# Performance work log

Hardware: AMD Instinct MI355X
Metric: run time of the kernel (lower is better)

## Reference

```python
import jax, jax.numpy as jnp
import numpy as np

N = 512          # Cartesian grid size (nRead)
C = 16           # n_coils
K = 262144       # n non-uniform k-space samples (~512 spokes x 512 readouts)


def setup_inputs() -> dict:
    key = jax.random.key(0)
    ks = jax.random.split(key, 6)
    x_real = jax.random.normal(ks[0], (C, K), jnp.float32)
    x_imag = jax.random.normal(ks[1], (C, K), jnp.float32)
    csm_real = jax.random.normal(ks[2], (C, N, N), jnp.float32)
    csm_imag = jax.random.normal(ks[3], (C, N, N), jnp.float32)
    # normalized k-space coordinates in [-0.5, 0.5)
    traj = jax.random.uniform(ks[4], (K, 2), jnp.float32, -0.5, 0.5)
    # density compensation weights (positive)
    dcf = jax.random.uniform(ks[5], (K,), jnp.float32)
    return dict(x_real=x_real, x_imag=x_imag, csm_real=csm_real,
                csm_imag=csm_imag, traj=traj, dcf=dcf)


def reference(x_real, x_imag, csm_real, csm_imag, traj, dcf):
    # Adjoint gridding NUFFT with density compensation + coil-sensitivity combine.
    # 1) density-compensate the multicoil non-Cartesian samples
    x = (x_real + 1j * x_imag) * dcf                      # [C, K] complex64
    # 2) grid (scatter-add) onto the Cartesian k-space grid (nearest-cell gridding)
    t = jax.lax.stop_gradient(traj)
    idx = jnp.round((t + 0.5) * N).astype(jnp.int32) % N  # [K, 2]
    iy, ix = idx[:, 0], idx[:, 1]
    grid = jnp.zeros((C, N, N), jnp.complex64).at[:, iy, ix].add(x)
    # 3) centered inverse FFT to image space (adjoint of DFT, scaled by N^2)
    img = jnp.fft.fftshift(
        jnp.fft.ifft2(jnp.fft.ifftshift(grid, axes=(-2, -1)), axes=(-2, -1)),
        axes=(-2, -1)) * (N * N)                          # [C, N, N]
    # 4) coil combine with conjugate sensitivity maps
    csm = csm_real + 1j * csm_imag
    out = jnp.sum(jnp.conj(csm) * img, axis=0)            # [N, N] complex64
    # return real/imag stacked, with batch dim (mimics numpy2tensor add_batch_dim)
    return jnp.stack([out.real, out.imag])[None]          # [1, 2, N, N]
```

## Files before the change

kernel.cpp:

```cpp
#include <hip/hip_runtime.h>
#include <math.h>

#define N 512
#define NN (N * N)
#define C 16
#define K 262144
#define LOG2N 9
#define NCOL 8

#define SK(e) ((e) + ((e) >> 4))
#define LROW 544


__global__ __launch_bounds__(256) void prep_hist_kernel(const float2* __restrict__ traj,
                                                        const float* __restrict__ dcf,
                                                        int* __restrict__ cell,
                                                        float* __restrict__ sdcf,
                                                        int* __restrict__ count) {
    int k = blockIdx.x * 256 + threadIdx.x;
    float2 t = traj[k];
    int iy = __float2int_rn((t.x + 0.5f) * (float)N) & (N - 1);
    int ix = __float2int_rn((t.y + 0.5f) * (float)N) & (N - 1);
    int cl = iy * N + ix;
    cell[k] = cl;
    float s = ((iy + ix) & 1) ? -1.0f : 1.0f;
    sdcf[k] = dcf[k] * s;
    atomicAdd(&count[cl], 1);
}

__global__ __launch_bounds__(256) void scan_reduce_kernel(const int* __restrict__ count,
                                                          int* __restrict__ bsum) {
    __shared__ int sd[256];
    int t = threadIdx.x;
    const int4* c4 = (const int4*)count;
    int4 v = c4[blockIdx.x * 256 + t];
    sd[t] = v.x + v.y + v.z + v.w;
    __syncthreads();
    for (int d = 128; d > 0; d >>= 1) {
        if (t < d) sd[t] += sd[t + d];
        __syncthreads();
    }
    if (t == 0) bsum[blockIdx.x] = sd[0];
}

__global__ __launch_bounds__(256) void scan_top_kernel(const int* __restrict__ bsum,
                                                       int* __restrict__ boffs,
                                                       int* __restrict__ offs) {
    __shared__ int sd[256];
    int t = threadIdx.x;
    int v = bsum[t];
    sd[t] = v;
    __syncthreads();
    for (int d = 1; d < 256; d <<= 1) {
        int tmp = (t >= d) ? sd[t - d] : 0;
        __syncthreads();
        sd[t] += tmp;
        __syncthreads();
    }
    boffs[t] = sd[t] - v;
    if (t == 0) offs[NN] = K;
}

__global__ __launch_bounds__(256) void scan_final_kernel(const int* __restrict__ count,
                                                         const int* __restrict__ boffs,
                                                         int* __restrict__ offs,
                                                         int* __restrict__ cursor) {
    __shared__ int sd[256];
    int t = threadIdx.x;
    int base_idx = blockIdx.x * 256 + t;
    const int4* c4 = (const int4*)count;
    int4 v = c4[base_idx];
    int s = v.x + v.y + v.z + v.w;
    sd[t] = s;
    __syncthreads();
    for (int d = 1; d < 256; d <<= 1) {
        int tmp = (t >= d) ? sd[t - d] : 0;
        __syncthreads();
        sd[t] += tmp;
        __syncthreads();
    }
    int base = boffs[blockIdx.x] + sd[t] - s;
    int4 o;
    o.x = base;
    o.y = base + v.x;
    o.z = base + v.x + v.y;
    o.w = base + v.x + v.y + v.z;
    ((int4*)offs)[base_idx] = o;
    ((int4*)cursor)[base_idx] = o;
}

__global__ __launch_bounds__(256) void payload_kernel(const float* __restrict__ xr,
                                                      const float* __restrict__ xi,
                                                      const int* __restrict__ cell,
                                                      const float* __restrict__ sdcf,
                                                      int* __restrict__ cursor,
                                                      float2* __restrict__ payA,
                                                      float2* __restrict__ payB) {
    __shared__ float tR[256][17];
    __shared__ float tI[256][17];
    __shared__ int   sp[256];
    __shared__ float sw[256];
    int t = threadIdx.x;
    int k0 = blockIdx.x * 256;
#pragma unroll
    for (int c = 0; c < C; ++c) {
        tR[t][c] = xr[(size_t)c * K + k0 + t];
        tI[t][c] = xi[(size_t)c * K + k0 + t];
    }
    int cl = cell[k0 + t];
    float w = sdcf[k0 + t];
    int p = atomicAdd(&cursor[cl], 1);
    sp[t] = p;
    sw[t] = w;
    __syncthreads();
    int sg = t >> 3, l = t & 7;
    for (int j = sg; j < 256; j += 32) {
        int pp = sp[j];
        float ww = sw[j];
        payA[(size_t)pp * 8 + l] = make_float2(tR[j][l] * ww,     tI[j][l] * ww);
        payB[(size_t)pp * 8 + l] = make_float2(tR[j][8 + l] * ww, tI[j][8 + l] * ww);
    }
}

__global__ __launch_bounds__(256) void build8_kernel(const int* __restrict__ offs,
                                                     const float4* __restrict__ payA4,
                                                     const float4* __restrict__ payB4,
                                                     float2* __restrict__ grid) {
    __shared__ float4 lds[4][LROW];
    int bid = blockIdx.x;
    int h = bid & 1;
    int r = bid >> 1;
    int t = threadIdx.x;
    int w = t >> 6;
    int l = t & 63;
    const float4* pay = h ? payB4 : payA4;
    const int* ro = offs + r * N;

#pragma unroll
    for (int it = 0; it < 8; ++it) {
        int col = l + (it << 6);
        int s = ro[col];
        int e = ro[col + 1];
        float4 acc = make_float4(0.f, 0.f, 0.f, 0.f);
        for (int p = s; p < e; ++p) {
            float4 v = pay[(size_t)p * 4 + w];
            acc.x += v.x; acc.y += v.y; acc.z += v.z; acc.w += v.w;
        }
        int bc = (int)(__brev((unsigned)col) >> (32 - LOG2N));
        lds[w][SK(bc)] = acc;
    }
    asm volatile("s_waitcnt lgkmcnt(0)" ::: "memory");

    for (int s = 1; s <= LOG2N; ++s) {
        int half = 1 << (s - 1);
        int m = half << 1;
#pragma unroll
        for (int i = 0; i < 4; ++i) {
            int b = l + (i << 6);
            int j = b & (half - 1);
            int grp = b >> (s - 1);
            int p1 = grp * m + j;
            int p2 = p1 + half;
            float ang = 6.283185307179586f * (float)j / (float)m;
            float sn, cs;
            __sincosf(ang, &sn, &cs);
            float4 v = lds[w][SK(p2)];
            float4 u = lds[w][SK(p1)];
            float tr0 = cs * v.x - sn * v.y;
            float ti0 = cs * v.y + sn * v.x;
            float tr1 = cs * v.z - sn * v.w;
            float ti1 = cs * v.w + sn * v.z;
            lds[w][SK(p2)] = make_float4(u.x - tr0, u.y - ti0, u.z - tr1, u.w - ti1);
            lds[w][SK(p1)] = make_float4(u.x + tr0, u.y + ti0, u.z + tr1, u.w + ti1);
        }
        asm volatile("s_waitcnt lgkmcnt(0)" ::: "memory");
    }

    int c0 = h * 8 + (w << 1);
    float2* g0 = grid + (size_t)c0 * NN + (size_t)r * N;
    float2* g1 = grid + (size_t)(c0 + 1) * NN + (size_t)r * N;
    for (int i = l; i < N; i += 64) {
        float4 v = lds[w][SK(i)];
        g0[i] = make_float2(v.x, v.y);
        g1[i] = make_float2(v.z, v.w);
    }
}

__global__ __launch_bounds__(256) void colfft_kernel(float2* __restrict__ grid) {
    __shared__ float sr[N * NCOL];
    __shared__ float si[N * NCOL];
    int blk = blockIdx.x;
    int c = blk >> 6;
    int cg = blk & 63;
    float2* base = grid + (size_t)c * NN + cg * NCOL;
    int t = threadIdx.x;

    for (int e = t; e < N * NCOL; e += 256) {
        int row = e >> 3, col = e & 7;
        float2 v = base[(size_t)row * N + col];
        sr[e] = v.x; si[e] = v.y;
    }
    __syncthreads();

    int col = t & 7;
    int tg = t >> 3;
    for (int i = tg; i < N; i += 32) {
        int j = __brev((unsigned)i) >> (32 - LOG2N);
        if (j > i) {
            int a1 = i * NCOL + col, a2 = j * NCOL + col;
            float a = sr[a1]; sr[a1] = sr[a2]; sr[a2] = a;
            float b = si[a1]; si[a1] = si[a2]; si[a2] = b;
        }
    }
    __syncthreads();

    for (int s = 1; s <= LOG2N; ++s) {
        int half = 1 << (s - 1);
        int m = half << 1;
        for (int b = tg; b < 256; b += 32) {
            int j = b & (half - 1);
            int grp = b >> (s - 1);
            int p1 = grp * m + j;
            int p2 = p1 + half;
            float ang = 6.283185307179586f * (float)j / (float)m;
            float sn, cs;
            __sincosf(ang, &sn, &cs);
            int a1 = p1 * NCOL + col, a2 = p2 * NCOL + col;
            float xr2 = sr[a2], xi2 = si[a2];
            float tr = cs * xr2 - sn * xi2;
            float ti = cs * xi2 + sn * xr2;
            float ur = sr[a1], ui = si[a1];
            sr[a2] = ur - tr; si[a2] = ui - ti;
            sr[a1] = ur + tr; si[a1] = ui + ti;
        }
        __syncthreads();
    }

    for (int e = t; e < N * NCOL; e += 256) {
        int row = e >> 3, col2 = e & 7;
        base[(size_t)row * N + col2] = make_float2(sr[e], si[e]);
    }
}

__global__ __launch_bounds__(256) void combine_kernel(const float* __restrict__ csr,
                                                      const float* __restrict__ csi,
                                                      const float2* __restrict__ grid,
                                                      float* __restrict__ out) {
    int pix = blockIdx.x * 256 + threadIdx.x;
    int ny = pix >> LOG2N, nx = pix & (N - 1);
    float ar = 0.f, ai = 0.f;
#pragma unroll
    for (int c = 0; c < C; ++c) {
        float2 uv = grid[(size_t)c * NN + pix];
        float a = csr[c * NN + pix];
        float b = csi[c * NN + pix];
        ar += a * uv.x + b * uv.y;
        ai += a * uv.y - b * uv.x;
    }
    float s = ((ny + nx) & 1) ? -1.f : 1.f;
    out[pix] = s * ar;
    out[NN + pix] = s * ai;
}

extern "C" void kernel_launch(void* const* d_in, const int* in_sizes, int n_in,
                              void* d_out, int out_size, void* d_ws, size_t ws_size,
                              hipStream_t stream) {
    const float* x_real   = (const float*)d_in[0];
    const float* x_imag   = (const float*)d_in[1];
    const float* csm_real = (const float*)d_in[2];
    const float* csm_imag = (const float*)d_in[3];
    const float2* traj    = (const float2*)d_in[4];
    const float* dcf      = (const float*)d_in[5];
    float* out = (float*)d_out;

    char* ws = (char*)d_ws;
    size_t o = 0;
    float* grid  = (float*)(ws + o); o += (size_t)C * NN * 2 * sizeof(float);
    int*   cell  = (int*)(ws + o);   o += (size_t)K * sizeof(int);
    float* sdcf  = (float*)(ws + o); o += (size_t)K * sizeof(float);
    int*   count = (int*)(ws + o);   o += (size_t)NN * sizeof(int);
    int*   offs  = (int*)(ws + o);   o += ((size_t)NN + 4) * sizeof(int);
    int*   cursor= (int*)(ws + o);   o += (size_t)NN * sizeof(int);
    float2* payA = (float2*)(ws + o); o += (size_t)K * 8 * sizeof(float2);
    float2* payB = (float2*)(ws + o); o += (size_t)K * 8 * sizeof(float2);
    int*   bsum  = (int*)(ws + o);   o += 256 * sizeof(int);
    int*   boffs = (int*)(ws + o);   o += 256 * sizeof(int);

    (void)hipMemsetAsync(count, 0, (size_t)NN * sizeof(int), stream);

    prep_hist_kernel<<<K / 256, 256, 0, stream>>>(traj, dcf, cell, sdcf, count);
    scan_reduce_kernel<<<256, 256, 0, stream>>>(count, bsum);
    scan_top_kernel<<<1, 256, 0, stream>>>(bsum, boffs, offs);
    scan_final_kernel<<<256, 256, 0, stream>>>(count, boffs, offs, cursor);
    payload_kernel<<<K / 256, 256, 0, stream>>>(x_real, x_imag, cell, sdcf, cursor, payA, payB);
    build8_kernel<<<N * 2, 256, 0, stream>>>(offs, (const float4*)payA, (const float4*)payB, (float2*)grid);
    colfft_kernel<<<C * (N / NCOL), 256, 0, stream>>>((float2*)grid);
    combine_kernel<<<NN / 256, 256, 0, stream>>>(csm_real, csm_imag, (float2*)grid, out);
}
```

Before: 215.9 us.

## Fuse histogram and scan with grid barrier, merge column FFT with coil combine

Merges histogram and the three scan kernels into one persistent 256-block kernel synchronised by a global atomic barrier. The column FFT is fused with the coil-sensitivity combine, so the FFT result is never written back to the grid before combining. The payload moves to a single interleaved 16-coil buffer, and the build kernel preloads its row offsets and first samples. These cut launches and a full grid round-trip, but the grid barrier relies on all 256 blocks being co-resident, and the fused kernel runs only 256 blocks that each loop over four coils serially.

```diff
diff --git a/kernel.cpp b/kernel.cpp
--- a/kernel.cpp
+++ b/kernel.cpp
@@ -6,50 +6,52 @@
 #define C 16
 #define K 262144
 #define LOG2N 9
-#define NCOL 8
 
 #define SK(e) ((e) + ((e) >> 4))
 #define LROW 544
 
 
-__global__ __launch_bounds__(256) void prep_hist_kernel(const float2* __restrict__ traj,
-                                                        const float* __restrict__ dcf,
-                                                        int* __restrict__ cell,
-                                                        float* __restrict__ sdcf,
-                                                        int* __restrict__ count) {
-    int k = blockIdx.x * 256 + threadIdx.x;
-    float2 t = traj[k];
-    int iy = __float2int_rn((t.x + 0.5f) * (float)N) & (N - 1);
-    int ix = __float2int_rn((t.y + 0.5f) * (float)N) & (N - 1);
-    int cl = iy * N + ix;
-    cell[k] = cl;
-    float s = ((iy + ix) & 1) ? -1.0f : 1.0f;
-    sdcf[k] = dcf[k] * s;
-    atomicAdd(&count[cl], 1);
-}
-
-__global__ __launch_bounds__(256) void scan_reduce_kernel(const int* __restrict__ count,
-                                                          int* __restrict__ bsum) {
+__device__ __forceinline__ void gridbar(int* bar, int target) {
+    __syncthreads();
+    if (threadIdx.x == 0) {
+        __threadfence();
+        __hip_atomic_fetch_add(bar, 1, __ATOMIC_ACQ_REL, __HIP_MEMORY_SCOPE_AGENT);
+        while (__hip_atomic_load(bar, __ATOMIC_ACQUIRE, __HIP_MEMORY_SCOPE_AGENT) < target) {
+            __builtin_amdgcn_s_sleep(8);
+        }
+        __threadfence();
+    }
+    __syncthreads();
+}
+
+__global__ __launch_bounds__(256) void scan_all_kernel(const float2* __restrict__ traj,
+                                                       const float* __restrict__ dcf,
+                                                       int* __restrict__ cell,
+                                                       float* __restrict__ sdcf,
+                                                       int* __restrict__ count,
+                                                       int* __restrict__ offs,
+                                                       int* __restrict__ cursor,
+                                                       int* __restrict__ chunk_sum,
+                                                       int* __restrict__ bar) {
     __shared__ int sd[256];
     int t = threadIdx.x;
-    const int4* c4 = (const int4*)count;
-    int4 v = c4[blockIdx.x * 256 + t];
-    sd[t] = v.x + v.y + v.z + v.w;
-    __syncthreads();
-    for (int d = 128; d > 0; d >>= 1) {
-        if (t < d) sd[t] += sd[t + d];
-        __syncthreads();
-    }
-    if (t == 0) bsum[blockIdx.x] = sd[0];
-}
-
-__global__ __launch_bounds__(256) void scan_top_kernel(const int* __restrict__ bsum,
-                                                       int* __restrict__ boffs,
-                                                       int* __restrict__ offs) {
-    __shared__ int sd[256];
-    int t = threadIdx.x;
-    int v = bsum[t];
-    sd[t] = v;
+    int b = blockIdx.x;
+
+    for (int i = b * 256 + t; i < K; i += 256 * 256) {
+        float2 tr = traj[i];
+        int iy = __float2int_rn((tr.x + 0.5f) * (float)N) & (N - 1);
+        int ix = __float2int_rn((tr.y + 0.5f) * (float)N) & (N - 1);
+        int cl = iy * N + ix;
+        cell[i] = cl;
+        float s = ((iy + ix) & 1) ? -1.0f : 1.0f;
+        sdcf[i] = dcf[i] * s;
+        atomicAdd(&count[cl], 1);
+    }
+    gridbar(bar, 256);
+
+    int4 c4 = ((const int4*)count)[b * 256 + t];
+    int tsum = c4.x + c4.y + c4.z + c4.w;
+    sd[t] = tsum;
     __syncthreads();
     for (int d = 1; d < 256; d <<= 1) {
         int tmp = (t >= d) ? sd[t - d] : 0;
@@ -57,36 +59,25 @@
         sd[t] += tmp;
         __syncthreads();
     }
-    boffs[t] = sd[t] - v;
-    if (t == 0) offs[NN] = K;
-}
-
-__global__ __launch_bounds__(256) void scan_final_kernel(const int* __restrict__ count,
-                                                         const int* __restrict__ boffs,
-                                                         int* __restrict__ offs,
-                                                         int* __restrict__ cursor) {
-    __shared__ int sd[256];
-    int t = threadIdx.x;
-    int base_idx = blockIdx.x * 256 + t;
-    const int4* c4 = (const int4*)count;
-    int4 v = c4[base_idx];
-    int s = v.x + v.y + v.z + v.w;
-    sd[t] = s;
-    __syncthreads();
-    for (int d = 1; d < 256; d <<= 1) {
-        int tmp = (t >= d) ? sd[t - d] : 0;
-        __syncthreads();
-        sd[t] += tmp;
-        __syncthreads();
-    }
-    int base = boffs[blockIdx.x] + sd[t] - s;
+    int incl = sd[t];
+    int epre = incl - tsum;
+    if (t == 255) chunk_sum[b] = incl;
+    gridbar(bar, 512);
+
+    __syncthreads();
+    sd[t] = (t < 256) ? chunk_sum[t] : 0;
+    __syncthreads();
+    int gbase = 0;
+    for (int j = 0; j < b; ++j) gbase += sd[j];
+    int base = gbase + epre;
     int4 o;
     o.x = base;
-    o.y = base + v.x;
-    o.z = base + v.x + v.y;
-    o.w = base + v.x + v.y + v.z;
-    ((int4*)offs)[base_idx] = o;
-    ((int4*)cursor)[base_idx] = o;
+    o.y = base + c4.x;
+    o.z = base + c4.x + c4.y;
+    o.w = base + c4.x + c4.y + c4.z;
+    ((int4*)offs)[b * 256 + t] = o;
+    ((int4*)cursor)[b * 256 + t] = o;
+    if (b == 255 && t == 255) offs[NN] = K;
 }
 
 __global__ __launch_bounds__(256) void payload_kernel(const float* __restrict__ xr,
@@ -94,8 +85,7 @@
                                                       const int* __restrict__ cell,
                                                       const float* __restrict__ sdcf,
                                                       int* __restrict__ cursor,
-                                                      float2* __restrict__ payA,
-                                                      float2* __restrict__ payB) {
+                                                      float2* __restrict__ pay) {
     __shared__ float tR[256][17];
     __shared__ float tI[256][17];
     __shared__ int   sp[256];
@@ -109,22 +99,19 @@
     }
     int cl = cell[k0 + t];
     float w = sdcf[k0 + t];
-    int p = atomicAdd(&cursor[cl], 1);
-    sp[t] = p;
+    sp[t] = atomicAdd(&cursor[cl], 1);
     sw[t] = w;
     __syncthreads();
-    int sg = t >> 3, l = t & 7;
-    for (int j = sg; j < 256; j += 32) {
+    int sg = t >> 4, l = t & 15;
+    for (int j = sg; j < 256; j += 16) {
         int pp = sp[j];
         float ww = sw[j];
-        payA[(size_t)pp * 8 + l] = make_float2(tR[j][l] * ww,     tI[j][l] * ww);
-        payB[(size_t)pp * 8 + l] = make_float2(tR[j][8 + l] * ww, tI[j][8 + l] * ww);
+        pay[(size_t)pp * 16 + l] = make_float2(tR[j][l] * ww, tI[j][l] * ww);
     }
 }
 
 __global__ __launch_bounds__(256) void build8_kernel(const int* __restrict__ offs,
-                                                     const float4* __restrict__ payA4,
-                                                     const float4* __restrict__ payB4,
+                                                     const float4* __restrict__ pay4,
                                                      float2* __restrict__ grid) {
     __shared__ float4 lds[4][LROW];
     int bid = blockIdx.x;
@@ -133,19 +120,30 @@
     int t = threadIdx.x;
     int w = t >> 6;
     int l = t & 63;
-    const float4* pay = h ? payB4 : payA4;
+    int q = h * 4 + w;
     const int* ro = offs + r * N;
 
+    int sv[8], ev[8];
 #pragma unroll
     for (int it = 0; it < 8; ++it) {
         int col = l + (it << 6);
-        int s = ro[col];
-        int e = ro[col + 1];
-        float4 acc = make_float4(0.f, 0.f, 0.f, 0.f);
-        for (int p = s; p < e; ++p) {
-            float4 v = pay[(size_t)p * 4 + w];
-            acc.x += v.x; acc.y += v.y; acc.z += v.z; acc.w += v.w;
-        }
+        sv[it] = ro[col];
+        ev[it] = ro[col + 1];
+    }
+    float4 vv[8];
+#pragma unroll
+    for (int it = 0; it < 8; ++it) {
+        vv[it] = make_float4(0.f, 0.f, 0.f, 0.f);
+        if (sv[it] < ev[it]) vv[it] = pay4[(size_t)sv[it] * 8 + q];
+    }
+#pragma unroll
+    for (int it = 0; it < 8; ++it) {
+        float4 acc = vv[it];
+        for (int p = sv[it] + 1; p < ev[it]; ++p) {
+            float4 v2 = pay4[(size_t)p * 8 + q];
+            acc.x += v2.x; acc.y += v2.y; acc.z += v2.z; acc.w += v2.w;
+        }
+        int col = l + (it << 6);
         int bc = (int)(__brev((unsigned)col) >> (32 - LOG2N));
         lds[w][SK(bc)] = acc;
     }
@@ -156,9 +154,9 @@
         int m = half << 1;
 #pragma unroll
         for (int i = 0; i < 4; ++i) {
-            int b = l + (i << 6);
-            int j = b & (half - 1);
-            int grp = b >> (s - 1);
+            int b2 = l + (i << 6);
+            int j = b2 & (half - 1);
+            int grp = b2 >> (s - 1);
             int p1 = grp * m + j;
             int p2 = p1 + half;
             float ang = 6.283185307179586f * (float)j / (float)m;
@@ -176,7 +174,7 @@
         asm volatile("s_waitcnt lgkmcnt(0)" ::: "memory");
     }
 
-    int c0 = h * 8 + (w << 1);
+    int c0 = q * 2;
     float2* g0 = grid + (size_t)c0 * NN + (size_t)r * N;
     float2* g1 = grid + (size_t)(c0 + 1) * NN + (size_t)r * N;
     for (int i = l; i < N; i += 64) {
@@ -186,80 +184,99 @@
     }
 }
 
-__global__ __launch_bounds__(256) void colfft_kernel(float2* __restrict__ grid) {
-    __shared__ float sr[N * NCOL];
-    __shared__ float si[N * NCOL];
-    int blk = blockIdx.x;
-    int c = blk >> 6;
-    int cg = blk & 63;
-    float2* base = grid + (size_t)c * NN + cg * NCOL;
+__global__ __launch_bounds__(256) void colfft_combine_kernel(const float2* __restrict__ grid,
+                                                             const float* __restrict__ csr,
+                                                             const float* __restrict__ csi,
+                                                             float* __restrict__ out) {
+    __shared__ float4 lds[4][LROW];
+    int cp = blockIdx.x;
     int t = threadIdx.x;
-
-    for (int e = t; e < N * NCOL; e += 256) {
-        int row = e >> 3, col = e & 7;
-        float2 v = base[(size_t)row * N + col];
-        sr[e] = v.x; si[e] = v.y;
-    }
-    __syncthreads();
-
-    int col = t & 7;
-    int tg = t >> 3;
-    for (int i = tg; i < N; i += 32) {
-        int j = __brev((unsigned)i) >> (32 - LOG2N);
-        if (j > i) {
-            int a1 = i * NCOL + col, a2 = j * NCOL + col;
-            float a = sr[a1]; sr[a1] = sr[a2]; sr[a2] = a;
-            float b = si[a1]; si[a1] = si[a2]; si[a2] = b;
-        }
-    }
-    __syncthreads();
-
-    for (int s = 1; s <= LOG2N; ++s) {
-        int half = 1 << (s - 1);
-        int m = half << 1;
-        for (int b = tg; b < 256; b += 32) {
-            int j = b & (half - 1);
-            int grp = b >> (s - 1);
-            int p1 = grp * m + j;
-            int p2 = p1 + half;
-            float ang = 6.283185307179586f * (float)j / (float)m;
-            float sn, cs;
-            __sincosf(ang, &sn, &cs);
-            int a1 = p1 * NCOL + col, a2 = p2 * NCOL + col;
-            float xr2 = sr[a2], xi2 = si[a2];
-            float tr = cs * xr2 - sn * xi2;
-            float ti = cs * xi2 + sn * xr2;
-            float ur = sr[a1], ui = si[a1];
-            sr[a2] = ur - tr; si[a2] = ui - ti;
-            sr[a1] = ur + tr; si[a1] = ui + ti;
+    int w = t >> 6;
+    int l = t & 63;
+    int colb = cp * 2;
+
+    float4 acc[8];
+#pragma unroll
+    for (int j = 0; j < 8; ++j) acc[j] = make_float4(0.f, 0.f, 0.f, 0.f);
+
+    for (int ci = 0; ci < 4; ++ci) {
+        int c = w + ci * 4;
+        const float2* g = grid + (size_t)c * NN + colb;
+#pragma unroll
+        for (int j = 0; j < 8; ++j) {
+            int row = l + (j << 6);
+            float2 a = g[(size_t)row * N];
+            float2 bv = g[(size_t)row * N + 1];
+            int br = (int)(__brev((unsigned)row) >> (32 - LOG2N));
+            lds[w][SK(br)] = make_float4(a.x, a.y, bv.x, bv.y);
+        }
+        asm volatile("s_waitcnt lgkmcnt(0)" ::: "memory");
+
+        for (int s = 1; s <= LOG2N; ++s) {
+            int half = 1 << (s - 1);
+            int m = half << 1;
+#pragma unroll
+            for (int i = 0; i < 4; ++i) {
+                int b2 = l + (i << 6);
+                int j = b2 & (half - 1);
+                int grp = b2 >> (s - 1);
+                int p1 = grp * m + j;
+                int p2 = p1 + half;
+                float ang = 6.283185307179586f * (float)j / (float)m;
+                float sn, cs;
+                __sincosf(ang, &sn, &cs);
+                float4 v = lds[w][SK(p2)];
+                float4 u = lds[w][SK(p1)];
+                float tr0 = cs * v.x - sn * v.y;
+                float ti0 = cs * v.y + sn * v.x;
+                float tr1 = cs * v.z - sn * v.w;
+                float ti1 = cs * v.w + sn * v.z;
+                lds[w][SK(p2)] = make_float4(u.x - tr0, u.y - ti0, u.z - tr1, u.w - ti1);
+                lds[w][SK(p1)] = make_float4(u.x + tr0, u.y + ti0, u.z + tr1, u.w + ti1);
+            }
+            asm volatile("s_waitcnt lgkmcnt(0)" ::: "memory");
+        }
+
+        const float* cr = csr + (size_t)c * NN + colb;
+        const float* cim = csi + (size_t)c * NN + colb;
+#pragma unroll
+        for (int j = 0; j < 8; ++j) {
+            int row = l + (j << 6);
+            float4 v = lds[w][SK(row)];
+            float2 a2 = *(const float2*)(cr + (size_t)row * N);
+            float2 b2 = *(const float2*)(cim + (size_t)row * N);
+            acc[j].x += a2.x * v.x + b2.x * v.y;
+            acc[j].y += a2.x * v.y - b2.x * v.x;
+            acc[j].z += a2.y * v.z + b2.y * v.w;
+            acc[j].w += a2.y * v.w - b2.y * v.z;
+        }
+        asm volatile("s_waitcnt lgkmcnt(0)" ::: "memory");
+    }
+
+    __syncthreads();
+    for (int ww = 0; ww < 4; ++ww) {
+        if (w == ww) {
+#pragma unroll
+            for (int j = 0; j < 8; ++j) {
+                int row = l + (j << 6);
+                if (ww == 0) {
+                    lds[0][SK(row)] = acc[j];
+                } else {
+                    float4 u = lds[0][SK(row)];
+                    u.x += acc[j].x; u.y += acc[j].y; u.z += acc[j].z; u.w += acc[j].w;
+                    lds[0][SK(row)] = u;
+                }
+            }
         }
         __syncthreads();
     }
-
-    for (int e = t; e < N * NCOL; e += 256) {
-        int row = e >> 3, col2 = e & 7;
-        base[(size_t)row * N + col2] = make_float2(sr[e], si[e]);
-    }
-}
-
-__global__ __launch_bounds__(256) void combine_kernel(const float* __restrict__ csr,
-                                                      const float* __restrict__ csi,
-                                                      const float2* __restrict__ grid,
-                                                      float* __restrict__ out) {
-    int pix = blockIdx.x * 256 + threadIdx.x;
-    int ny = pix >> LOG2N, nx = pix & (N - 1);
-    float ar = 0.f, ai = 0.f;
-#pragma unroll
-    for (int c = 0; c < C; ++c) {
-        float2 uv = grid[(size_t)c * NN + pix];
-        float a = csr[c * NN + pix];
-        float b = csi[c * NN + pix];
-        ar += a * uv.x + b * uv.y;
-        ai += a * uv.y - b * uv.x;
-    }
-    float s = ((ny + nx) & 1) ? -1.f : 1.f;
-    out[pix] = s * ar;
-    out[NN + pix] = s * ai;
+    for (int row = t; row < N; row += 256) {
+        float4 v = lds[0][SK(row)];
+        float s0 = ((row + colb) & 1) ? -1.f : 1.f;
+        float s1 = -s0;
+        *(float2*)(out + (size_t)row * N + colb)      = make_float2(s0 * v.x, s1 * v.z);
+        *(float2*)(out + NN + (size_t)row * N + colb) = make_float2(s0 * v.y, s1 * v.w);
+    }
 }
 
 extern "C" void kernel_launch(void* const* d_in, const int* in_sizes, int n_in,
@@ -279,21 +296,16 @@
     int*   cell  = (int*)(ws + o);   o += (size_t)K * sizeof(int);
     float* sdcf  = (float*)(ws + o); o += (size_t)K * sizeof(float);
     int*   count = (int*)(ws + o);   o += (size_t)NN * sizeof(int);
+    int*   bar   = (int*)(ws + o);   o += 64;
     int*   offs  = (int*)(ws + o);   o += ((size_t)NN + 4) * sizeof(int);
     int*   cursor= (int*)(ws + o);   o += (size_t)NN * sizeof(int);
-    float2* payA = (float2*)(ws + o); o += (size_t)K * 8 * sizeof(float2);
-    float2* payB = (float2*)(ws + o); o += (size_t)K * 8 * sizeof(float2);
-    int*   bsum  = (int*)(ws + o);   o += 256 * sizeof(int);
-    int*   boffs = (int*)(ws + o);   o += 256 * sizeof(int);
-
-    (void)hipMemsetAsync(count, 0, (size_t)NN * sizeof(int), stream);
-
-    prep_hist_kernel<<<K / 256, 256, 0, stream>>>(traj, dcf, cell, sdcf, count);
-    scan_reduce_kernel<<<256, 256, 0, stream>>>(count, bsum);
-    scan_top_kernel<<<1, 256, 0, stream>>>(bsum, boffs, offs);
-    scan_final_kernel<<<256, 256, 0, stream>>>(count, boffs, offs, cursor);
-    payload_kernel<<<K / 256, 256, 0, stream>>>(x_real, x_imag, cell, sdcf, cursor, payA, payB);
-    build8_kernel<<<N * 2, 256, 0, stream>>>(offs, (const float4*)payA, (const float4*)payB, (float2*)grid);
-    colfft_kernel<<<C * (N / NCOL), 256, 0, stream>>>((float2*)grid);
-    combine_kernel<<<NN / 256, 256, 0, stream>>>(csm_real, csm_imag, (float2*)grid, out);
-}
+    float2* pay  = (float2*)(ws + o); o += (size_t)K * 16 * sizeof(float2);
+    int*   chunk_sum = (int*)(ws + o); o += 256 * sizeof(int);
+
+    (void)hipMemsetAsync(count, 0, (size_t)NN * sizeof(int) + 64, stream);
+
+    scan_all_kernel<<<256, 256, 0, stream>>>(traj, dcf, cell, sdcf, count, offs, cursor, chunk_sum, bar);
+    payload_kernel<<<K / 256, 256, 0, stream>>>(x_real, x_imag, cell, sdcf, cursor, pay);
+    build8_kernel<<<N * 2, 256, 0, stream>>>(offs, (const float4*)pay, (float2*)grid);
+    colfft_combine_kernel<<<256, 256, 0, stream>>>((const float2*)grid, csm_real, csm_imag, out);
+}
```

New measurement: 320.2 us. +48.3%, slower.
